# Optimization experiments

Measured on AMD Instinct MI355X. Metric: run time of the kernel, lower is better.

The kernel has to match this reference:

```python
import jax, jax.numpy as jnp
import numpy as np

C = 1.0          # Poincare ball curvature
H = 8            # num_heads
EPS = 1e-15
DELTA = 1e-7
SC = np.sqrt(C)  # sqrt curvature


def _norm(x):
    return jnp.sqrt(jnp.clip(jnp.sum(x * x, -1, keepdims=True), 1e-15))


def mobius_add(x, y):
    xy = jnp.sum(x * y, -1, keepdims=True)
    x2 = jnp.sum(x * x, -1, keepdims=True)
    y2 = jnp.sum(y * y, -1, keepdims=True)
    num = (1 + 2 * C * xy + C * y2) * x + (1 - C * x2) * y
    den = 1 + 2 * C * xy + C * C * x2 * y2
    return num / (den + EPS)


def mobius_matvec(W, x):
    xn = _norm(x)
    mx = x @ W.T
    mxn = _norm(mx)
    arg = jnp.clip(SC * xn, None, 1 - 1e-5)
    return jnp.tanh(mxn / xn * jnp.arctanh(arg)) * mx / (mxn * SC)


def logmap0(x):
    xn = _norm(x)
    return jnp.arctanh(jnp.clip(SC * xn, None, 1 - 1e-5)) * x / (SC * xn)


def expmap0(u):
    un = _norm(u)
    return jnp.tanh(SC * un) * u / (SC * un)


def hyp_linear(W, b, x):
    return mobius_add(mobius_matvec(W, x), b)


def setup_inputs() -> dict:
    key = jax.random.key(0)
    ks = jax.random.split(key, 5)
    B, S, E = 2, 512, 256
    x = jax.random.normal(ks[0], (B, S, E), jnp.float32) * 0.02  # inside unit ball
    scale = float(np.sqrt(6.0 / (E + E)))  # xavier uniform bound
    Wq = jax.random.uniform(ks[1], (E, E), jnp.float32, -scale, scale)
    Wk = jax.random.uniform(ks[2], (E, E), jnp.float32, -scale, scale)
    Wv = jax.random.uniform(ks[3], (E, E), jnp.float32, -scale, scale)
    Wo = jax.random.uniform(ks[4], (E, E), jnp.float32, -scale, scale)
    z = jnp.zeros((E,), jnp.float32)
    head_scaling = jnp.ones((H, 1, 1), jnp.float32)
    return {"x": x, "Wq": Wq, "bq": z, "Wk": Wk, "bk": z, "Wv": Wv, "bv": z,
            "Wo": Wo, "bo": z, "head_scaling": head_scaling}


def reference(x, Wq, bq, Wk, bk, Wv, bv, Wo, bo, head_scaling):
    B, S, E = x.shape
    D = E // H
    q = hyp_linear(Wq, bq, x).reshape(B, S, H, D).transpose(0, 2, 1, 3)  # (B,H,S,D)
    k = hyp_linear(Wk, bk, x).reshape(B, S, H, D).transpose(0, 2, 1, 3)
    v = hyp_linear(Wv, bv, x).reshape(B, S, H, D).transpose(0, 2, 1, 3)
    max_norm = (1 - 1e-5) / SC
    q = jnp.minimum(q, max_norm)  # elementwise clamp_max, faithful to source
    k = jnp.minimum(k, max_norm)
    qn = C * jnp.sum(q * q, -1)[..., :, None]   # (B,H,Sq,1)
    kn = C * jnp.sum(k * k, -1)[..., None, :]   # (B,H,1,Sk)
    # pairwise mobius_add(-k, q): (B,H,Sq,Sk,D)
    diff = mobius_add(-k[:, :, None, :, :], q[:, :, :, None, :])
    dn = C * jnp.sum(diff * diff, -1)           # (B,H,Sq,Sk)
    denom = (1 - qn) * (1 - kn) + EPS
    a = jnp.maximum(1 + 2 * dn / denom, 1 + DELTA)
    dist = jnp.log(a + jnp.sqrt(a * a - 1))     # acosh
    scores = -dist / (head_scaling * np.sqrt(D))
    w = jax.nn.softmax(scores, -1)
    out = expmap0(jnp.einsum('bhqk,bhkd->bhqd', w, logmap0(v)))
    out = out.transpose(0, 2, 1, 3).reshape(B, S, E)
    return hyp_linear(Wo, bo, out)
```

## Files before the change

kernel.cpp:

```cpp
#include <hip/hip_runtime.h>
#include <math.h>

#define Ec 256
#define Sc 512
#define Bc 2
#define Hc 8
#define Dc 32
#define MAXNORM (1.0f - 1e-5f)
#define NEc (Bc * Sc * Ec)
#define KSPLIT 4
#define NROWS (Bc * Hc * Sc)

__device__ __forceinline__ float fullWaveSum(float v) {
#pragma unroll
  for (int m = 32; m >= 1; m >>= 1) v += __shfl_xor(v, m, 64);
  return v;
}
__device__ __forceinline__ float halfWaveSum(float v) {
#pragma unroll
  for (int m = 16; m >= 1; m >>= 1) v += __shfl_xor(v, m, 64);
  return v;
}
__device__ __forceinline__ float atanh_fast(float z) {
  return 0.5f * __logf((1.0f + z) / (1.0f - z));
}
__device__ __forceinline__ float tanh_fast(float a) {
  float e = __expf(-2.0f * a);
  return (1.0f - e) / (1.0f + e);
}

__global__ __launch_bounds__(128) void gemm_xwt(
    const float* __restrict__ X,
    const float* __restrict__ W0, const float* __restrict__ W1,
    const float* __restrict__ W2,
    float* __restrict__ O0, float* __restrict__ O1, float* __restrict__ O2) {
  const int tid = threadIdx.x;
  const int bx = blockIdx.x;
  const int by = blockIdx.y;
  const int kz = blockIdx.z;
  const int mat = by >> 2;
  const int cb0 = (by & 3) * 64;
  const int rb0 = bx * 32;
  const int kk = kz * 64;
  const float* __restrict__ W = (mat == 0) ? W0 : (mat == 1) ? W1 : W2;
  float* __restrict__ O = ((mat == 0) ? O0 : (mat == 1) ? O1 : O2) + (size_t)kz * NEc;

  __shared__ float Xs[64][36];
  __shared__ float Ws[64][68];

  const int f4 = tid & 15;
  const int sub = tid >> 4;
  const int ty = tid >> 4;
  const int tx = tid & 15;

#pragma unroll
  for (int i = 0; i < 4; ++i) {
    int row = sub + i * 8;
    float4 v = *(const float4*)&X[(size_t)(rb0 + row) * Ec + kk + f4 * 4];
    Xs[f4 * 4 + 0][row] = v.x;
    Xs[f4 * 4 + 1][row] = v.y;
    Xs[f4 * 4 + 2][row] = v.z;
    Xs[f4 * 4 + 3][row] = v.w;
  }
#pragma unroll
  for (int i = 0; i < 8; ++i) {
    int col = sub + i * 8;
    float4 v = *(const float4*)&W[(size_t)(cb0 + col) * Ec + kk + f4 * 4];
    Ws[f4 * 4 + 0][col] = v.x;
    Ws[f4 * 4 + 1][col] = v.y;
    Ws[f4 * 4 + 2][col] = v.z;
    Ws[f4 * 4 + 3][col] = v.w;
  }
  __syncthreads();

  float acc[4][4];
#pragma unroll
  for (int i = 0; i < 4; ++i)
#pragma unroll
    for (int j = 0; j < 4; ++j) acc[i][j] = 0.f;

#pragma unroll 8
  for (int k = 0; k < 64; ++k) {
    float4 a = *(const float4*)&Xs[k][ty * 4];
    float4 b = *(const float4*)&Ws[k][tx * 4];
    float av[4] = {a.x, a.y, a.z, a.w};
    float bv[4] = {b.x, b.y, b.z, b.w};
#pragma unroll
    for (int i = 0; i < 4; ++i)
#pragma unroll
      for (int j = 0; j < 4; ++j) acc[i][j] = fmaf(av[i], bv[j], acc[i][j]);
  }
#pragma unroll
  for (int i = 0; i < 4; ++i) {
    float4 o = make_float4(acc[i][0], acc[i][1], acc[i][2], acc[i][3]);
    *(float4*)&O[(size_t)(rb0 + ty * 4 + i) * Ec + cb0 + tx * 4] = o;
  }
}

__global__ __launch_bounds__(256) void qkv_stats(
    const float* __restrict__ x,
    const float* __restrict__ mxq, const float* __restrict__ mxk,
    const float* __restrict__ mxv,
    const float* __restrict__ bq, const float* __restrict__ bk,
    const float* __restrict__ bv,
    float* __restrict__ qo, float* __restrict__ ko, float* __restrict__ lvo,
    float* __restrict__ qno, float* __restrict__ kno) {
  const int t = threadIdx.x;
  const int row = blockIdx.x;
  const int b = row >> 9;
  const int s = row & (Sc - 1);
  const size_t idx = (size_t)row * Ec + t;
  const float xv = x[idx];
  float mq = 0.f, mk = 0.f, mv = 0.f;
#pragma unroll
  for (int p = 0; p < KSPLIT; ++p) {
    mq += mxq[idx + (size_t)p * NEc];
    mk += mxk[idx + (size_t)p * NEc];
    mv += mxv[idx + (size_t)p * NEc];
  }
  const float bb[3] = {bq[t], bk[t], bv[t]};
  const float mvals[3] = {mq, mk, mv};

  float vals[10] = {xv * xv,
                    mq * mq, mq * bb[0], bb[0] * bb[0],
                    mk * mk, mk * bb[1], bb[1] * bb[1],
                    mv * mv, mv * bb[2], bb[2] * bb[2]};
  __shared__ float red[10][4];
  __shared__ float fin[10];
#pragma unroll
  for (int i = 0; i < 10; ++i) {
    float v = fullWaveSum(vals[i]);
    if ((t & 63) == 0) red[i][t >> 6] = v;
  }
  __syncthreads();
  if (t < 10) fin[t] = red[t][0] + red[t][1] + red[t][2] + red[t][3];
  __syncthreads();

  const float x2 = fin[0];
  const float xn = sqrtf(fmaxf(x2, 1e-15f));
  const float at = atanh_fast(fminf(xn, MAXNORM));
  const int h = t >> 5;

#pragma unroll
  for (int m = 0; m < 3; ++m) {
    float mx2 = fin[1 + 3 * m];
    float mxb = fin[2 + 3 * m];
    float b2 = fin[3 + 3 * m];
    float mxn = sqrtf(fmaxf(mx2, 1e-15f));
    float scl = tanh_fast((mxn / xn) * at) / mxn;
    float mvv = scl * mvals[m];
    float X2 = scl * scl * mx2;
    float XY = scl * mxb;
    float numc = 1.0f + 2.0f * XY + b2;
    float den = 1.0f + 2.0f * XY + X2 * b2 + 1e-15f;
    float res = (numc * mvv + (1.0f - X2) * bb[m]) / den;
    if (m < 2) {
      res = fminf(res, MAXNORM);
      float s2 = halfWaveSum(res * res);
      if (m == 0) {
        qo[idx] = res;
        if ((t & 31) == 0) qno[(b * Hc + h) * Sc + s] = s2;
      } else {
        ko[idx] = res;
        if ((t & 31) == 0) kno[(b * Hc + h) * Sc + s] = s2;
      }
    } else {
      float vn2 = halfWaveSum(res * res);
      float vn = sqrtf(fmaxf(vn2, 1e-15f));
      float f = atanh_fast(fminf(vn, MAXNORM)) / vn;
      lvo[idx] = f * res;
    }
  }
}

__global__ __launch_bounds__(256) void score_kernel(
    const float* __restrict__ q, const float* __restrict__ k,
    const float* __restrict__ qn, const float* __restrict__ kn,
    const float* __restrict__ hs, float* __restrict__ P) {
  const int tid = threadIdx.x;
  const int sk0 = blockIdx.x * 64;
  const int sq0 = blockIdx.y * 64;
  const int bh = blockIdx.z;
  const int b = bh >> 3;
  const int h = bh & 7;

  __shared__ float Qs[64][32];
  __shared__ float Ks[64][32];

#pragma unroll
  for (int i = 0; i < 2; ++i) {
    int qi = tid + i * 256;
    int r = qi >> 3;
    int fd = qi & 7;
    int fsw = fd ^ ((r >> 2) & 7);
    float4 v = *(const float4*)&q[(size_t)(b * Sc + sq0 + r) * Ec + h * Dc + fd * 4];
    *(float4*)&Qs[r][fsw * 4] = v;
    float4 w = *(const float4*)&k[(size_t)(b * Sc + sk0 + r) * Ec + h * Dc + fd * 4];
    *(float4*)&Ks[r][fsw * 4] = w;
  }
  __syncthreads();

  const int ty = tid >> 4;
  const int tx = tid & 15;

  float acc[4][4];
#pragma unroll
  for (int i = 0; i < 4; ++i)
#pragma unroll
    for (int j = 0; j < 4; ++j) acc[i][j] = 0.f;

#pragma unroll
  for (int fd = 0; fd < 8; ++fd) {
    const int qsw = (fd ^ (ty & 7)) * 4;
    const int ksw = (fd ^ (tx & 7)) * 4;
    float4 a[4], bb[4];
#pragma unroll
    for (int i = 0; i < 4; ++i) a[i] = *(const float4*)&Qs[ty * 4 + i][qsw];
#pragma unroll
    for (int j = 0; j < 4; ++j) bb[j] = *(const float4*)&Ks[tx * 4 + j][ksw];
#pragma unroll
    for (int i = 0; i < 4; ++i)
#pragma unroll
      for (int j = 0; j < 4; ++j) {
        acc[i][j] = fmaf(a[i].x, bb[j].x, acc[i][j]);
        acc[i][j] = fmaf(a[i].y, bb[j].y, acc[i][j]);
        acc[i][j] = fmaf(a[i].z, bb[j].z, acc[i][j]);
        acc[i][j] = fmaf(a[i].w, bb[j].w, acc[i][j]);
      }
  }

  const float sinv = -1.0f / (hs[h] * sqrtf((float)Dc));
  float qnv[4], knv[4];
#pragma unroll
  for (int i = 0; i < 4; ++i) qnv[i] = qn[bh * Sc + sq0 + ty * 4 + i];
#pragma unroll
  for (int j = 0; j < 4; ++j) knv[j] = kn[bh * Sc + sk0 + tx * 4 + j];

#pragma unroll
  for (int i = 0; i < 4; ++i) {
    const float q2 = qnv[i];
    const float omq = 1.0f - q2;
    float4 o;
    float po[4];
#pragma unroll
    for (int j = 0; j < 4; ++j) {
      const float k2 = knv[j];
      const float kq = acc[i][j];
      const float omk = 1.0f - k2;
      float s2x2 = fmaf(-4.0f, kq, 2.0f * k2 + 2.0f * q2);
      float dden = fmaf(k2, q2, fmaf(-2.0f, kq, 1.0f)) + 1e-15f;
      float Pd = fmaf(dden, omk * omq, 1e-20f);
      float rp = __builtin_amdgcn_rcpf(Pd);
      float tt = fmaxf(s2x2 * rp, 1e-7f);
      float z = (1.0f + tt) + sqrtf(fmaf(tt, tt, tt + tt));
      po[j] = __builtin_amdgcn_exp2f(sinv * __builtin_amdgcn_logf(z));
    }
    o.x = po[0]; o.y = po[1]; o.z = po[2]; o.w = po[3];
    *(float4*)&P[((size_t)bh * Sc + sq0 + ty * 4 + i) * Sc + sk0 + tx * 4] = o;
  }
}

__global__ __launch_bounds__(256) void pv_kernel(
    const float* __restrict__ P, const float* __restrict__ lv,
    float* __restrict__ out) {
  const int tid = threadIdx.x;
  const int sq0 = blockIdx.x * 16;
  const int bh = blockIdx.y;
  const int b = bh >> 3;
  const int h = bh & 7;
  const int js = tid >> 5;
  const int rg = (tid >> 3) & 3;
  const int dq = tid & 7;

  __shared__ float Ps[16][68];
  __shared__ float lvs[64][36];
  __shared__ float accm[16][8][32];
  __shared__ float lsb[16][9];

  float4 acc[4];
#pragma unroll
  for (int i = 0; i < 4; ++i) acc[i] = make_float4(0.f, 0.f, 0.f, 0.f);
  float lsum4[4] = {0.f, 0.f, 0.f, 0.f};

#pragma unroll 1
  for (int t = 0; t < 8; ++t) {
    const int j0g = t * 64;
    {
      int pr = tid >> 4, pc = tid & 15;
      *(float4*)&Ps[pr][pc * 4] =
          *(const float4*)&P[((size_t)bh * Sc + sq0 + pr) * Sc + j0g + pc * 4];
#pragma unroll
      for (int i = 0; i < 2; ++i) {
        int qi = tid + i * 256;
        int lr = qi >> 3, lc = qi & 7;
        *(float4*)&lvs[lr][lc * 4] =
            *(const float4*)&lv[(size_t)(b * Sc + j0g + lr) * Ec + h * Dc + lc * 4];
      }
    }
    __syncthreads();

#pragma unroll
    for (int j4 = 0; j4 < 2; ++j4) {
      const int j0 = js * 8 + j4 * 4;
      float4 p[4], l[4];
#pragma unroll
      for (int i = 0; i < 4; ++i) p[i] = *(const float4*)&Ps[rg * 4 + i][j0];
#pragma unroll
      for (int c = 0; c < 4; ++c) l[c] = *(const float4*)&lvs[j0 + c][dq * 4];
#pragma unroll
      for (int i = 0; i < 4; ++i) {
        lsum4[i] += (p[i].x + p[i].y) + (p[i].z + p[i].w);
        acc[i].x = fmaf(p[i].x, l[0].x, acc[i].x);
        acc[i].y = fmaf(p[i].x, l[0].y, acc[i].y);
        acc[i].z = fmaf(p[i].x, l[0].z, acc[i].z);
        acc[i].w = fmaf(p[i].x, l[0].w, acc[i].w);
        acc[i].x = fmaf(p[i].y, l[1].x, acc[i].x);
        acc[i].y = fmaf(p[i].y, l[1].y, acc[i].y);
        acc[i].z = fmaf(p[i].y, l[1].z, acc[i].z);
        acc[i].w = fmaf(p[i].y, l[1].w, acc[i].w);
        acc[i].x = fmaf(p[i].z, l[2].x, acc[i].x);
        acc[i].y = fmaf(p[i].z, l[2].y, acc[i].y);
        acc[i].z = fmaf(p[i].z, l[2].z, acc[i].z);
        acc[i].w = fmaf(p[i].z, l[2].w, acc[i].w);
        acc[i].x = fmaf(p[i].w, l[3].x, acc[i].x);
        acc[i].y = fmaf(p[i].w, l[3].y, acc[i].y);
        acc[i].z = fmaf(p[i].w, l[3].z, acc[i].z);
        acc[i].w = fmaf(p[i].w, l[3].w, acc[i].w);
      }
    }
    __syncthreads();
  }

#pragma unroll
  for (int i = 0; i < 4; ++i)
    *(float4*)&accm[rg * 4 + i][js][dq * 4] = acc[i];
  if (dq == 0) {
#pragma unroll
    for (int i = 0; i < 4; ++i) lsb[rg * 4 + i][js] = lsum4[i];
  }
  __syncthreads();

  const int r2 = tid >> 4;
  const int dd = tid & 15;
  float o0 = 0.f, o1 = 0.f, ls = 0.f;
#pragma unroll
  for (int g = 0; g < 8; ++g) {
    float2 a2 = *(const float2*)&accm[r2][g][dd * 2];
    o0 += a2.x;
    o1 += a2.y;
    ls += lsb[r2][g];
  }
  const float li = 1.0f / ls;
  o0 *= li;
  o1 *= li;
  float un2 = fmaf(o0, o0, o1 * o1);
#pragma unroll
  for (int m = 8; m >= 1; m >>= 1) un2 += __shfl_xor(un2, m, 16);
  float un = sqrtf(fmaxf(un2, 1e-15f));
  float f = tanh_fast(un) / un;
  float2 ov = make_float2(o0 * f, o1 * f);
  *(float2*)&out[(size_t)(b * Sc + sq0 + r2) * Ec + h * Dc + dd * 2] = ov;
}

__global__ __launch_bounds__(256) void proj_stats(
    const float* __restrict__ xin, const float* __restrict__ mx,
    const float* __restrict__ bo, float* __restrict__ out) {
  const int t = threadIdx.x;
  const int row = blockIdx.x;
  const size_t idx = (size_t)row * Ec + t;
  const float xv = xin[idx];
  float m = 0.f;
#pragma unroll
  for (int p = 0; p < KSPLIT; ++p) m += mx[idx + (size_t)p * NEc];
  const float bb = bo[t];
  float vals[4] = {xv * xv, m * m, m * bb, bb * bb};
  __shared__ float red[4][4];
  __shared__ float fin[4];
#pragma unroll
  for (int i = 0; i < 4; ++i) {
    float v = fullWaveSum(vals[i]);
    if ((t & 63) == 0) red[i][t >> 6] = v;
  }
  __syncthreads();
  if (t < 4) fin[t] = red[t][0] + red[t][1] + red[t][2] + red[t][3];
  __syncthreads();

  float x2 = fin[0], mx2 = fin[1], mxb = fin[2], b2 = fin[3];
  float xn = sqrtf(fmaxf(x2, 1e-15f));
  float mxn = sqrtf(fmaxf(mx2, 1e-15f));
  float scl = tanh_fast((mxn / xn) * atanh_fast(fminf(xn, MAXNORM))) / mxn;
  float mvv = scl * m;
  float X2 = scl * scl * mx2;
  float XY = scl * mxb;
  float numc = 1.0f + 2.0f * XY + b2;
  float den = 1.0f + 2.0f * XY + X2 * b2 + 1e-15f;
  out[idx] = (numc * mvv + (1.0f - X2) * bb) / den;
}

extern "C" void kernel_launch(void* const* d_in, const int* in_sizes, int n_in,
                              void* d_out, int out_size, void* d_ws, size_t ws_size,
                              hipStream_t stream) {
  (void)in_sizes; (void)n_in; (void)out_size; (void)ws_size;
  const float* x  = (const float*)d_in[0];
  const float* Wq = (const float*)d_in[1];
  const float* bq = (const float*)d_in[2];
  const float* Wk = (const float*)d_in[3];
  const float* bk = (const float*)d_in[4];
  const float* Wv = (const float*)d_in[5];
  const float* bv = (const float*)d_in[6];
  const float* Wo = (const float*)d_in[7];
  const float* bo = (const float*)d_in[8];
  const float* hs = (const float*)d_in[9];

  float* ws = (float*)d_ws;
  const int NE = NEc;
  const int NH = NROWS;
  float* mxq = ws;
  float* mxk = mxq + KSPLIT * NE;
  float* mxv = mxk + KSPLIT * NE;
  float* mxo = mxv + KSPLIT * NE;
  float* qb  = mxo + KSPLIT * NE;
  float* kb  = qb + NE;
  float* lvb = kb + NE;
  float* aob = lvb + NE;
  float* qnb = aob + NE;
  float* knb = qnb + NH;
  float* Pb  = knb + NH;

  const int M = Bc * Sc;

  gemm_xwt<<<dim3(M / 32, 12, KSPLIT), 128, 0, stream>>>(x, Wq, Wk, Wv, mxq, mxk, mxv);
  qkv_stats<<<M, 256, 0, stream>>>(x, mxq, mxk, mxv, bq, bk, bv,
                                   qb, kb, lvb, qnb, knb);
  score_kernel<<<dim3(8, 8, 16), 256, 0, stream>>>(qb, kb, qnb, knb, hs, Pb);
  pv_kernel<<<dim3(32, 16), 256, 0, stream>>>(Pb, lvb, aob);
  gemm_xwt<<<dim3(M / 32, 4, KSPLIT), 128, 0, stream>>>(aob, Wo, Wo, Wo, mxo, mxo, mxo);
  proj_stats<<<M, 256, 0, stream>>>(aob, mxo, bo, (float*)d_out);
}
```

Before: 125.0 us.

## Fuse score and PV kernels into one attention kernel; halve GEMM K-split

Merges the score kernel and the PV kernel into one attention kernel. Each block computes a 32-row query tile against 256-key tiles and keeps the probabilities in shared memory, so the full score matrix is no longer written to and read back from global memory. Separately, the GEMM K-split drops from 4 to 2, with each block looping over two 64-wide K chunks, which cuts partial-sum traffic. The fused kernel launches only 256 blocks of 512 threads and uses large shared memory (roughly 110KB), which may limit occupancy and parallelism.

```diff
diff --git a/kernel.cpp b/kernel.cpp
--- a/kernel.cpp
+++ b/kernel.cpp
@@ -8,7 +8,7 @@
 #define Dc 32
 #define MAXNORM (1.0f - 1e-5f)
 #define NEc (Bc * Sc * Ec)
-#define KSPLIT 4
+#define KSPLIT 2
 #define NROWS (Bc * Hc * Sc)
 
 __device__ __forceinline__ float fullWaveSum(float v) {
@@ -41,7 +41,6 @@
   const int mat = by >> 2;
   const int cb0 = (by & 3) * 64;
   const int rb0 = bx * 32;
-  const int kk = kz * 64;
   const float* __restrict__ W = (mat == 0) ? W0 : (mat == 1) ? W1 : W2;
   float* __restrict__ O = ((mat == 0) ? O0 : (mat == 1) ? O1 : O2) + (size_t)kz * NEc;
 
@@ -53,42 +52,44 @@
   const int ty = tid >> 4;
   const int tx = tid & 15;
 
-#pragma unroll
-  for (int i = 0; i < 4; ++i) {
-    int row = sub + i * 8;
-    float4 v = *(const float4*)&X[(size_t)(rb0 + row) * Ec + kk + f4 * 4];
-    Xs[f4 * 4 + 0][row] = v.x;
-    Xs[f4 * 4 + 1][row] = v.y;
-    Xs[f4 * 4 + 2][row] = v.z;
-    Xs[f4 * 4 + 3][row] = v.w;
-  }
-#pragma unroll
-  for (int i = 0; i < 8; ++i) {
-    int col = sub + i * 8;
-    float4 v = *(const float4*)&W[(size_t)(cb0 + col) * Ec + kk + f4 * 4];
-    Ws[f4 * 4 + 0][col] = v.x;
-    Ws[f4 * 4 + 1][col] = v.y;
-    Ws[f4 * 4 + 2][col] = v.z;
-    Ws[f4 * 4 + 3][col] = v.w;
-  }
-  __syncthreads();
-
   float acc[4][4];
 #pragma unroll
   for (int i = 0; i < 4; ++i)
 #pragma unroll
     for (int j = 0; j < 4; ++j) acc[i][j] = 0.f;
 
+  for (int kk = kz * 128; kk < kz * 128 + 128; kk += 64) {
+    __syncthreads();
+#pragma unroll
+    for (int i = 0; i < 4; ++i) {
+      int row = sub + i * 8;
+      float4 v = *(const float4*)&X[(size_t)(rb0 + row) * Ec + kk + f4 * 4];
+      Xs[f4 * 4 + 0][row] = v.x;
+      Xs[f4 * 4 + 1][row] = v.y;
+      Xs[f4 * 4 + 2][row] = v.z;
+      Xs[f4 * 4 + 3][row] = v.w;
+    }
+#pragma unroll
+    for (int i = 0; i < 8; ++i) {
+      int col = sub + i * 8;
+      float4 v = *(const float4*)&W[(size_t)(cb0 + col) * Ec + kk + f4 * 4];
+      Ws[f4 * 4 + 0][col] = v.x;
+      Ws[f4 * 4 + 1][col] = v.y;
+      Ws[f4 * 4 + 2][col] = v.z;
+      Ws[f4 * 4 + 3][col] = v.w;
+    }
+    __syncthreads();
 #pragma unroll 8
-  for (int k = 0; k < 64; ++k) {
-    float4 a = *(const float4*)&Xs[k][ty * 4];
-    float4 b = *(const float4*)&Ws[k][tx * 4];
-    float av[4] = {a.x, a.y, a.z, a.w};
-    float bv[4] = {b.x, b.y, b.z, b.w};
-#pragma unroll
-    for (int i = 0; i < 4; ++i)
-#pragma unroll
-      for (int j = 0; j < 4; ++j) acc[i][j] = fmaf(av[i], bv[j], acc[i][j]);
+    for (int k = 0; k < 64; ++k) {
+      float4 a = *(const float4*)&Xs[k][ty * 4];
+      float4 b = *(const float4*)&Ws[k][tx * 4];
+      float av[4] = {a.x, a.y, a.z, a.w};
+      float bv[4] = {b.x, b.y, b.z, b.w};
+#pragma unroll
+      for (int i = 0; i < 4; ++i)
+#pragma unroll
+        for (int j = 0; j < 4; ++j) acc[i][j] = fmaf(av[i], bv[j], acc[i][j]);
+    }
   }
 #pragma unroll
   for (int i = 0; i < 4; ++i) {
@@ -173,135 +174,116 @@
   }
 }
 
-__global__ __launch_bounds__(256) void score_kernel(
+__global__ __launch_bounds__(512) void attn_fused(
     const float* __restrict__ q, const float* __restrict__ k,
-    const float* __restrict__ qn, const float* __restrict__ kn,
-    const float* __restrict__ hs, float* __restrict__ P) {
-  const int tid = threadIdx.x;
-  const int sk0 = blockIdx.x * 64;
-  const int sq0 = blockIdx.y * 64;
-  const int bh = blockIdx.z;
-  const int b = bh >> 3;
-  const int h = bh & 7;
-
-  __shared__ float Qs[64][32];
-  __shared__ float Ks[64][32];
-
-#pragma unroll
-  for (int i = 0; i < 2; ++i) {
-    int qi = tid + i * 256;
-    int r = qi >> 3;
-    int fd = qi & 7;
-    int fsw = fd ^ ((r >> 2) & 7);
-    float4 v = *(const float4*)&q[(size_t)(b * Sc + sq0 + r) * Ec + h * Dc + fd * 4];
-    *(float4*)&Qs[r][fsw * 4] = v;
-    float4 w = *(const float4*)&k[(size_t)(b * Sc + sk0 + r) * Ec + h * Dc + fd * 4];
-    *(float4*)&Ks[r][fsw * 4] = w;
-  }
-  __syncthreads();
-
-  const int ty = tid >> 4;
-  const int tx = tid & 15;
-
-  float acc[4][4];
-#pragma unroll
-  for (int i = 0; i < 4; ++i)
-#pragma unroll
-    for (int j = 0; j < 4; ++j) acc[i][j] = 0.f;
-
-#pragma unroll
-  for (int fd = 0; fd < 8; ++fd) {
-    const int qsw = (fd ^ (ty & 7)) * 4;
-    const int ksw = (fd ^ (tx & 7)) * 4;
-    float4 a[4], bb[4];
-#pragma unroll
-    for (int i = 0; i < 4; ++i) a[i] = *(const float4*)&Qs[ty * 4 + i][qsw];
-#pragma unroll
-    for (int j = 0; j < 4; ++j) bb[j] = *(const float4*)&Ks[tx * 4 + j][ksw];
-#pragma unroll
-    for (int i = 0; i < 4; ++i)
-#pragma unroll
-      for (int j = 0; j < 4; ++j) {
-        acc[i][j] = fmaf(a[i].x, bb[j].x, acc[i][j]);
-        acc[i][j] = fmaf(a[i].y, bb[j].y, acc[i][j]);
-        acc[i][j] = fmaf(a[i].z, bb[j].z, acc[i][j]);
-        acc[i][j] = fmaf(a[i].w, bb[j].w, acc[i][j]);
-      }
-  }
-
-  const float sinv = -1.0f / (hs[h] * sqrtf((float)Dc));
-  float qnv[4], knv[4];
-#pragma unroll
-  for (int i = 0; i < 4; ++i) qnv[i] = qn[bh * Sc + sq0 + ty * 4 + i];
-#pragma unroll
-  for (int j = 0; j < 4; ++j) knv[j] = kn[bh * Sc + sk0 + tx * 4 + j];
-
-#pragma unroll
-  for (int i = 0; i < 4; ++i) {
-    const float q2 = qnv[i];
-    const float omq = 1.0f - q2;
-    float4 o;
-    float po[4];
-#pragma unroll
-    for (int j = 0; j < 4; ++j) {
-      const float k2 = knv[j];
-      const float kq = acc[i][j];
-      const float omk = 1.0f - k2;
-      float s2x2 = fmaf(-4.0f, kq, 2.0f * k2 + 2.0f * q2);
-      float dden = fmaf(k2, q2, fmaf(-2.0f, kq, 1.0f)) + 1e-15f;
-      float Pd = fmaf(dden, omk * omq, 1e-20f);
-      float rp = __builtin_amdgcn_rcpf(Pd);
-      float tt = fmaxf(s2x2 * rp, 1e-7f);
-      float z = (1.0f + tt) + sqrtf(fmaf(tt, tt, tt + tt));
-      po[j] = __builtin_amdgcn_exp2f(sinv * __builtin_amdgcn_logf(z));
-    }
-    o.x = po[0]; o.y = po[1]; o.z = po[2]; o.w = po[3];
-    *(float4*)&P[((size_t)bh * Sc + sq0 + ty * 4 + i) * Sc + sk0 + tx * 4] = o;
-  }
-}
-
-__global__ __launch_bounds__(256) void pv_kernel(
-    const float* __restrict__ P, const float* __restrict__ lv,
+    const float* __restrict__ lv, const float* __restrict__ qn,
+    const float* __restrict__ kn, const float* __restrict__ hs,
     float* __restrict__ out) {
   const int tid = threadIdx.x;
-  const int sq0 = blockIdx.x * 16;
+  const int qt = blockIdx.x;
   const int bh = blockIdx.y;
   const int b = bh >> 3;
   const int h = bh & 7;
-  const int js = tid >> 5;
-  const int rg = (tid >> 3) & 3;
+  const int sq0 = qt * 32;
+
+  __shared__ float Qs[32][32];
+  __shared__ float Ks[256][32];
+  __shared__ float lvs[256][36];
+  __shared__ float Ps[32][260];
+  __shared__ float accm[32][8][32];
+  __shared__ float lsb[32][8];
+
+  const int ty = tid >> 6;
+  const int tx = tid & 63;
+  const int js = tid >> 6;
+  const int rg = (tid >> 3) & 7;
   const int dq = tid & 7;
 
-  __shared__ float Ps[16][68];
-  __shared__ float lvs[64][36];
-  __shared__ float accm[16][8][32];
-  __shared__ float lsb[16][9];
-
-  float4 acc[4];
-#pragma unroll
-  for (int i = 0; i < 4; ++i) acc[i] = make_float4(0.f, 0.f, 0.f, 0.f);
+  if (tid < 256) {
+    int r = tid >> 3, fd = tid & 7;
+    int fsw = fd ^ ((r >> 2) & 7);
+    *(float4*)&Qs[r][fsw * 4] =
+        *(const float4*)&q[(size_t)(b * Sc + sq0 + r) * Ec + h * Dc + fd * 4];
+  }
+  const float sinv = -1.0f / (hs[h] * sqrtf((float)Dc));
+  float qnv[4];
+#pragma unroll
+  for (int i = 0; i < 4; ++i) qnv[i] = qn[bh * Sc + sq0 + ty * 4 + i];
+
+  float4 oacc[4];
+#pragma unroll
+  for (int i = 0; i < 4; ++i) oacc[i] = make_float4(0.f, 0.f, 0.f, 0.f);
   float lsum4[4] = {0.f, 0.f, 0.f, 0.f};
 
 #pragma unroll 1
-  for (int t = 0; t < 8; ++t) {
-    const int j0g = t * 64;
-    {
-      int pr = tid >> 4, pc = tid & 15;
-      *(float4*)&Ps[pr][pc * 4] =
-          *(const float4*)&P[((size_t)bh * Sc + sq0 + pr) * Sc + j0g + pc * 4];
-#pragma unroll
-      for (int i = 0; i < 2; ++i) {
-        int qi = tid + i * 256;
-        int lr = qi >> 3, lc = qi & 7;
-        *(float4*)&lvs[lr][lc * 4] =
-            *(const float4*)&lv[(size_t)(b * Sc + j0g + lr) * Ec + h * Dc + lc * 4];
+  for (int kt = 0; kt < 2; ++kt) {
+    const int k0 = kt * 256;
+    __syncthreads();
+#pragma unroll
+    for (int i = 0; i < 4; ++i) {
+      int qi = tid + i * 512;
+      int r = qi >> 3, fd = qi & 7;
+      int fsw = fd ^ ((r >> 2) & 7);
+      *(float4*)&Ks[r][fsw * 4] =
+          *(const float4*)&k[(size_t)(b * Sc + k0 + r) * Ec + h * Dc + fd * 4];
+      *(float4*)&lvs[r][fd * 4] =
+          *(const float4*)&lv[(size_t)(b * Sc + k0 + r) * Ec + h * Dc + fd * 4];
+    }
+    float knv[4];
+#pragma unroll
+    for (int j = 0; j < 4; ++j) knv[j] = kn[bh * Sc + k0 + tx * 4 + j];
+    __syncthreads();
+
+    float acc[4][4];
+#pragma unroll
+    for (int i = 0; i < 4; ++i)
+#pragma unroll
+      for (int j = 0; j < 4; ++j) acc[i][j] = 0.f;
+#pragma unroll
+    for (int fd = 0; fd < 8; ++fd) {
+      const int qsw = (fd ^ (ty & 7)) * 4;
+      const int ksw = (fd ^ (tx & 7)) * 4;
+      float4 a[4], bb[4];
+#pragma unroll
+      for (int i = 0; i < 4; ++i) a[i] = *(const float4*)&Qs[ty * 4 + i][qsw];
+#pragma unroll
+      for (int j = 0; j < 4; ++j) bb[j] = *(const float4*)&Ks[tx * 4 + j][ksw];
+#pragma unroll
+      for (int i = 0; i < 4; ++i)
+#pragma unroll
+        for (int j = 0; j < 4; ++j) {
+          acc[i][j] = fmaf(a[i].x, bb[j].x, acc[i][j]);
+          acc[i][j] = fmaf(a[i].y, bb[j].y, acc[i][j]);
+          acc[i][j] = fmaf(a[i].z, bb[j].z, acc[i][j]);
+          acc[i][j] = fmaf(a[i].w, bb[j].w, acc[i][j]);
+        }
+    }
+#pragma unroll
+    for (int i = 0; i < 4; ++i) {
+      const float q2 = qnv[i];
+      const float omq = 1.0f - q2;
+      float po[4];
+#pragma unroll
+      for (int j = 0; j < 4; ++j) {
+        const float k2 = knv[j];
+        const float kq = acc[i][j];
+        const float omk = 1.0f - k2;
+        float s2x2 = fmaf(-4.0f, kq, 2.0f * k2 + 2.0f * q2);
+        float dden = fmaf(k2, q2, fmaf(-2.0f, kq, 1.0f)) + 1e-15f;
+        float Pd = fmaf(dden, omk * omq, 1e-20f);
+        float rp = __builtin_amdgcn_rcpf(Pd);
+        float tt = fmaxf(s2x2 * rp, 1e-7f);
+        float z = (1.0f + tt) + sqrtf(fmaf(tt, tt, tt + tt));
+        po[j] = __builtin_amdgcn_exp2f(sinv * __builtin_amdgcn_logf(z));
       }
+      float4 o4 = make_float4(po[0], po[1], po[2], po[3]);
+      *(float4*)&Ps[ty * 4 + i][tx * 4] = o4;
     }
     __syncthreads();
 
 #pragma unroll
-    for (int j4 = 0; j4 < 2; ++j4) {
-      const int j0 = js * 8 + j4 * 4;
+    for (int jq = 0; jq < 8; ++jq) {
+      const int j0 = js * 32 + jq * 4;
       float4 p[4], l[4];
 #pragma unroll
       for (int i = 0; i < 4; ++i) p[i] = *(const float4*)&Ps[rg * 4 + i][j0];
@@ -310,56 +292,57 @@
 #pragma unroll
       for (int i = 0; i < 4; ++i) {
         lsum4[i] += (p[i].x + p[i].y) + (p[i].z + p[i].w);
-        acc[i].x = fmaf(p[i].x, l[0].x, acc[i].x);
-        acc[i].y = fmaf(p[i].x, l[0].y, acc[i].y);
-        acc[i].z = fmaf(p[i].x, l[0].z, acc[i].z);
-        acc[i].w = fmaf(p[i].x, l[0].w, acc[i].w);
-        acc[i].x = fmaf(p[i].y, l[1].x, acc[i].x);
-        acc[i].y = fmaf(p[i].y, l[1].y, acc[i].y);
-        acc[i].z = fmaf(p[i].y, l[1].z, acc[i].z);
-        acc[i].w = fmaf(p[i].y, l[1].w, acc[i].w);
-        acc[i].x = fmaf(p[i].z, l[2].x, acc[i].x);
-        acc[i].y = fmaf(p[i].z, l[2].y, acc[i].y);
-        acc[i].z = fmaf(p[i].z, l[2].z, acc[i].z);
-        acc[i].w = fmaf(p[i].z, l[2].w, acc[i].w);
-        acc[i].x = fmaf(p[i].w, l[3].x, acc[i].x);
-        acc[i].y = fmaf(p[i].w, l[3].y, acc[i].y);
-        acc[i].z = fmaf(p[i].w, l[3].z, acc[i].z);
-        acc[i].w = fmaf(p[i].w, l[3].w, acc[i].w);
+        oacc[i].x = fmaf(p[i].x, l[0].x, oacc[i].x);
+        oacc[i].y = fmaf(p[i].x, l[0].y, oacc[i].y);
+        oacc[i].z = fmaf(p[i].x, l[0].z, oacc[i].z);
+        oacc[i].w = fmaf(p[i].x, l[0].w, oacc[i].w);
+        oacc[i].x = fmaf(p[i].y, l[1].x, oacc[i].x);
+        oacc[i].y = fmaf(p[i].y, l[1].y, oacc[i].y);
+        oacc[i].z = fmaf(p[i].y, l[1].z, oacc[i].z);
+        oacc[i].w = fmaf(p[i].y, l[1].w, oacc[i].w);
+        oacc[i].x = fmaf(p[i].z, l[2].x, oacc[i].x);
+        oacc[i].y = fmaf(p[i].z, l[2].y, oacc[i].y);
+        oacc[i].z = fmaf(p[i].z, l[2].z, oacc[i].z);
+        oacc[i].w = fmaf(p[i].z, l[2].w, oacc[i].w);
+        oacc[i].x = fmaf(p[i].w, l[3].x, oacc[i].x);
+        oacc[i].y = fmaf(p[i].w, l[3].y, oacc[i].y);
+        oacc[i].z = fmaf(p[i].w, l[3].z, oacc[i].z);
+        oacc[i].w = fmaf(p[i].w, l[3].w, oacc[i].w);
       }
     }
-    __syncthreads();
-  }
-
+  }
+
+  __syncthreads();
 #pragma unroll
   for (int i = 0; i < 4; ++i)
-    *(float4*)&accm[rg * 4 + i][js][dq * 4] = acc[i];
+    *(float4*)&accm[rg * 4 + i][js][dq * 4] = oacc[i];
   if (dq == 0) {
 #pragma unroll
     for (int i = 0; i < 4; ++i) lsb[rg * 4 + i][js] = lsum4[i];
   }
   __syncthreads();
 
-  const int r2 = tid >> 4;
-  const int dd = tid & 15;
-  float o0 = 0.f, o1 = 0.f, ls = 0.f;
-#pragma unroll
-  for (int g = 0; g < 8; ++g) {
-    float2 a2 = *(const float2*)&accm[r2][g][dd * 2];
-    o0 += a2.x;
-    o1 += a2.y;
-    ls += lsb[r2][g];
-  }
-  const float li = 1.0f / ls;
-  o0 *= li;
-  o1 *= li;
-  float un2 = fmaf(o0, o0, o1 * o1);
-#pragma unroll
-  for (int m = 8; m >= 1; m >>= 1) un2 += __shfl_xor(un2, m, 16);
-  float un = sqrtf(fmaxf(un2, 1e-15f));
-  float f = tanh_fast(un) / un;
-  float2 ov = make_float2(o0 * f, o1 * f);
-  *(float2*)&out[(size_t)(b * Sc + sq0 + r2) * Ec + h * Dc + dd * 2] = ov;
+  if (tid < 256) {
+    const int rw = tid >> 3;
+    const int d2 = tid & 7;
+    float4 o = make_float4(0.f, 0.f, 0.f, 0.f);
+    float ls = 0.f;
+#pragma unroll
+    for (int g = 0; g < 8; ++g) {
+      float4 a4 = *(const float4*)&accm[rw][g][d2 * 4];
+      o.x += a4.x; o.y += a4.y; o.z += a4.z; o.w += a4.w;
+      ls += lsb[rw][g];
+    }
+    const float li = 1.0f / ls;
+    o.x *= li; o.y *= li; o.z *= li; o.w *= li;
+    float un2 = fmaf(o.x, o.x, fmaf(o.y, o.y, fmaf(o.z, o.z, o.w * o.w)));
+#pragma unroll
+    for (int m = 4; m >= 1; m >>= 1) un2 += __shfl_xor(un2, m, 8);
+    float un = sqrtf(fmaxf(un2, 1e-15f));
+    float f = tanh_fast(un) / un;
+    float4 ov = make_float4(o.x * f, o.y * f, o.z * f, o.w * f);
+    *(float4*)&out[(size_t)(b * Sc + sq0 + rw) * Ec + h * Dc + d2 * 4] = ov;
+  }
 }
 
 __global__ __launch_bounds__(256) void proj_stats(
@@ -425,15 +408,13 @@
   float* aob = lvb + NE;
   float* qnb = aob + NE;
   float* knb = qnb + NH;
-  float* Pb  = knb + NH;
 
   const int M = Bc * Sc;
 
   gemm_xwt<<<dim3(M / 32, 12, KSPLIT), 128, 0, stream>>>(x, Wq, Wk, Wv, mxq, mxk, mxv);
   qkv_stats<<<M, 256, 0, stream>>>(x, mxq, mxk, mxv, bq, bk, bv,
                                    qb, kb, lvb, qnb, knb);
-  score_kernel<<<dim3(8, 8, 16), 256, 0, stream>>>(qb, kb, qnb, knb, hs, Pb);
-  pv_kernel<<<dim3(32, 16), 256, 0, stream>>>(Pb, lvb, aob);
+  attn_fused<<<dim3(16, 16), 512, 0, stream>>>(qb, kb, lvb, qnb, knb, hs, aob);
   gemm_xwt<<<dim3(M / 32, 4, KSPLIT), 128, 0, stream>>>(aob, Wo, Wo, Wo, mxo, mxo, mxo);
   proj_stats<<<M, 256, 0, stream>>>(aob, mxo, bo, (float*)d_out);
 }
```

After: 125.6 us. No clear change (+0.5%).
